# Optimization experiments

Measured on AMD Instinct MI355X. Metric: run time of the kernel, lower is better.

## Reference

```python
import jax, jax.numpy as jnp
import numpy as np

NUM_CLASSES = 2
THRESHOLD = 0.35
NEGPOS_RATIO = 7
VARIANCES = (0.1, 0.2)
B, P, O = 64, 16800, 64  # batch, num_priors, num_objs per image


def point_form(pr):
    # cxcywh -> xyxy
    return jnp.concatenate([pr[:, :2] - pr[:, 2:] / 2, pr[:, :2] + pr[:, 2:] / 2], axis=1)


def jaccard(a, b):
    # a: [A,4] xyxy, b: [Bx,4] xyxy -> IoU [A,Bx]
    lt = jnp.maximum(a[:, None, :2], b[None, :, :2])
    rb = jnp.minimum(a[:, None, 2:], b[None, :, 2:])
    wh = jnp.clip(rb - lt, 0.0)
    inter = wh[..., 0] * wh[..., 1]
    area_a = ((a[:, 2] - a[:, 0]) * (a[:, 3] - a[:, 1]))[:, None]
    area_b = ((b[:, 2] - b[:, 0]) * (b[:, 3] - b[:, 1]))[None, :]
    return inter / (area_a + area_b - inter)


def encode(matched, priors):
    # matched xyxy [P,4], priors cxcywh [P,4]
    g_cxcy = (matched[:, :2] + matched[:, 2:]) / 2 - priors[:, :2]
    g_cxcy = g_cxcy / (VARIANCES[0] * priors[:, 2:])
    g_wh = (matched[:, 2:] - matched[:, :2]) / priors[:, 2:]
    g_wh = jnp.log(g_wh) / VARIANCES[1]
    return jnp.concatenate([g_cxcy, g_wh], axis=1)


def encode_landm(matched, priors):
    # matched [P,10] -> [P,5,2]
    m = matched.reshape(-1, 5, 2)
    g = (m - priors[:, None, :2]) / (VARIANCES[0] * priors[:, None, 2:])
    return g.reshape(-1, 10)


def match_one(truths, labels, landms, priors):
    # truths [O,4], labels [O], landms [O,10]
    overlaps = jaccard(truths, point_form(priors))  # [O,P]
    best_prior_overlap = overlaps.max(axis=1)       # per-gt best IoU
    best_prior_idx = overlaps.argmax(axis=1)
    valid_gt = best_prior_overlap >= 0.2
    best_truth_overlap = overlaps.max(axis=0)       # per-prior best IoU
    best_truth_idx = overlaps.argmax(axis=0)
    # index_fill(2) only for valid gts (best_prior_idx_filter)
    bto = best_truth_overlap.at[best_prior_idx].set(
        jnp.where(valid_gt, 2.0, best_truth_overlap[best_prior_idx]))
    # ensure every gt keeps its best prior
    bti = best_truth_idx.at[best_prior_idx].set(jnp.arange(truths.shape[0]))
    matches = truths[bti]                  # [P,4]
    conf = labels[bti]                     # [P]
    conf = jnp.where(bto < THRESHOLD, 0.0, conf)
    loc = encode(matches, priors)
    landm = encode_landm(landms[bti], priors)
    return loc, conf, landm


def smooth_l1_sum(x, mask):
    ax = jnp.abs(x)
    v = jnp.where(ax < 1.0, 0.5 * ax * ax, ax - 0.5)
    return (v * mask).sum()


def setup_inputs() -> dict:
    key = jax.random.key(0)
    k1, k2, k3, k4, k5, k6, k7, k8 = jax.random.split(key, 8)
    loc_data = jax.random.normal(k1, (B, P, 4), jnp.float32)
    conf_data = jax.random.normal(k2, (B, P, NUM_CLASSES), jnp.float32)
    landm_data = jax.random.normal(k3, (B, P, 10), jnp.float32)
    # priors: cx,cy in (0,1), w,h in (0.02,0.22)
    cxy = jax.random.uniform(k4, (P, 2), jnp.float32)
    wh = jax.random.uniform(k5, (P, 2), jnp.float32) * 0.2 + 0.02
    priors = jnp.concatenate([cxy, wh], axis=1)
    # targets: valid corner boxes + landmarks + label in {1,-1}
    xy1 = jax.random.uniform(k6, (B, O, 2), jnp.float32) * 0.6
    bwh = jax.random.uniform(k7, (B, O, 2), jnp.float32) * 0.3 + 0.05
    boxes = jnp.concatenate([xy1, xy1 + bwh], axis=-1)
    lms = jax.random.uniform(k8, (B, O, 10), jnp.float32)
    lab = jnp.where(jax.random.uniform(jax.random.fold_in(key, 9), (B, O, 1)) < 0.3, -1.0, 1.0)
    targets = jnp.concatenate([boxes, lms, lab], axis=-1)
    return {"loc_data": loc_data, "conf_data": conf_data, "landm_data": landm_data,
            "priors": priors, "targets": targets}


def reference(loc_data, conf_data, landm_data, priors, targets):
    num = loc_data.shape[0]
    num_priors = priors.shape[0]
    truths = targets[:, :, :4]
    landms = targets[:, :, 4:14]
    labels = targets[:, :, -1]
    loc_t, conf_t, landm_t = jax.vmap(match_one, in_axes=(0, 0, 0, None))(
        truths, labels, landms, priors)  # [B,P,4], [B,P], [B,P,10]

    # landmark loss over conf_t > 0
    pos1 = conf_t > 0
    num_pos_landm = pos1.astype(jnp.int32).sum(axis=1, keepdims=True)
    N1 = jnp.maximum(num_pos_landm.sum().astype(jnp.float32), 1.0)
    loss_landm = smooth_l1_sum(landm_data - landm_t, pos1[..., None].astype(landm_data.dtype))

    # localization loss over conf_t != 0 ; conf_t[pos] = 1
    pos = conf_t != 0
    conf_t01 = jnp.where(pos, 1, 0)  # int {0,1}
    loss_l = smooth_l1_sum(loc_data - loc_t, pos[..., None].astype(loc_data.dtype))

    # hard negative mining on per-prior CE loss (global-max log_sum_exp, as in source)
    batch_conf = conf_data.reshape(-1, NUM_CLASSES)
    x_max = batch_conf.max()
    lse = jnp.log(jnp.exp(batch_conf - x_max).sum(axis=1, keepdims=True)) + x_max
    gathered = jnp.take_along_axis(batch_conf, conf_t01.reshape(-1, 1), axis=1)
    loss_c = (lse - gathered).reshape(num, -1)  # [B,P]; positives NOT zeroed (as in source)
    loss_idx = jnp.argsort(-loss_c, axis=1)
    idx_rank = jnp.argsort(loss_idx, axis=1)
    num_pos = pos.astype(jnp.int32).sum(axis=1, keepdims=True)  # [B,1]
    num_neg = jnp.minimum(NEGPOS_RATIO * num_pos, num_priors - 1)
    neg = idx_rank < num_neg  # [B,P]
    neg_pos = pos | neg

    # cross-entropy (sum) over selected pos+neg priors
    logp = jax.nn.log_softmax(conf_data, axis=-1)  # [B,P,C]
    ce = -jnp.take_along_axis(logp, conf_t01[..., None], axis=-1)[..., 0]
    loss_c_final = (ce * neg_pos.astype(ce.dtype)).sum()

    N = jnp.maximum(num_pos.sum().astype(jnp.float32), 1.0)
    return (loss_l / N, loss_c_final / N, loss_landm / N1)
```

## Files before the change

kernel.cpp:

```cpp
#include <hip/hip_runtime.h>
#include <math.h>

#define BN 64
#define PN 16800
#define ON 64
#define THRESH 0.35f
#define NEGPOS 7
#define GX 66
#define NBLK (BN * GX)
#define GXB 17
#define PT 4
#define TG 4

__device__ __forceinline__ unsigned f2key(float f) {
  unsigned u = __float_as_uint(f);
  return (u & 0x80000000u) ? ~u : (u | 0x80000000u);
}
__device__ __forceinline__ float key2f(unsigned k) {
  unsigned u = (k & 0x80000000u) ? (k & 0x7FFFFFFFu) : ~k;
  return __uint_as_float(u);
}
__device__ __forceinline__ float sl1(float d) {
  float a = fabsf(d);
  return (a < 1.f) ? 0.5f * a * a : a - 0.5f;
}

__global__ void k_best_truth(const float* __restrict__ priors,
                             const float* __restrict__ targets,
                             float* __restrict__ bto, int* __restrict__ bti) {
  int b = blockIdx.y;
  int tid = threadIdx.x;
  int base = blockIdx.x * 1024 + tid;

  __shared__ float4 tbox[ON];
  __shared__ float tarea[ON];
  if (tid < ON) {
    const float* tg = &targets[((long)b * ON + tid) * 15];
    float4 bx = make_float4(tg[0], tg[1], tg[2], tg[3]);
    tbox[tid] = bx;
    tarea[tid] = (bx.z - bx.x) * (bx.w - bx.y);
  }
  __syncthreads();

  float px1[PT], py1[PT], px2[PT], py2[PT], ab[PT];
  bool val[PT];
#pragma unroll
  for (int i = 0; i < PT; i++) {
    int p = base + 256 * i;
    val[i] = p < PN;
    float4 pr = reinterpret_cast<const float4*>(priors)[val[i] ? p : base];
    px1[i] = pr.x - pr.z * 0.5f; py1[i] = pr.y - pr.w * 0.5f;
    px2[i] = pr.x + pr.z * 0.5f; py2[i] = pr.y + pr.w * 0.5f;
    ab[i] = (px2[i] - px1[i]) * (py2[i] - py1[i]);
  }
  float bi[PT], bu[PT]; int id[PT];
#pragma unroll
  for (int i = 0; i < PT; i++) { bi[i] = -1.f; bu[i] = 1.f; id[i] = 0; }

#pragma unroll 4
  for (int t = 0; t < ON; t++) {
    float4 a = tbox[t];
    float aa = tarea[t];
#pragma unroll
    for (int i = 0; i < PT; i++) {
      float lx = fmaxf(a.x, px1[i]), ly = fmaxf(a.y, py1[i]);
      float rx = fminf(a.z, px2[i]), ry = fminf(a.w, py2[i]);
      float w = fmaxf(rx - lx, 0.f), h = fmaxf(ry - ly, 0.f);
      float inter = w * h;
      float uni = aa + ab[i] - inter;
      if (inter * bu[i] > bi[i] * uni) { bi[i] = inter; bu[i] = uni; id[i] = t; }
    }
  }
#pragma unroll
  for (int i = 0; i < PT; i++) {
    if (val[i]) {
      int p = base + 256 * i;
      bto[(long)b * PN + p] = bi[i] / bu[i];
      bti[(long)b * PN + p] = id[i];
    }
  }
}

__global__ void k_best_prior(const float* __restrict__ priors,
                             const float* __restrict__ targets,
                             float* __restrict__ bpo, int* __restrict__ bpi) {
  int bx = blockIdx.x;
  int b = bx >> 4;
  int t0 = (bx & 15) * TG;
  int tid = threadIdx.x;
  float ax1[TG], ay1[TG], ax2[TG], ay2[TG], area_a[TG];
#pragma unroll
  for (int i = 0; i < TG; i++) {
    const float* tg = &targets[((long)b * ON + t0 + i) * 15];
    ax1[i] = tg[0]; ay1[i] = tg[1]; ax2[i] = tg[2]; ay2[i] = tg[3];
    area_a[i] = (ax2[i] - ax1[i]) * (ay2[i] - ay1[i]);
  }
  float bi[TG], bu[TG]; int bp[TG];
#pragma unroll
  for (int i = 0; i < TG; i++) { bi[i] = -1.f; bu[i] = 1.f; bp[i] = 0x7FFFFFFF; }
  for (int p = tid; p < PN; p += 256) {
    float4 pr = reinterpret_cast<const float4*>(priors)[p];
    float px1 = pr.x - pr.z * 0.5f, py1 = pr.y - pr.w * 0.5f;
    float px2 = pr.x + pr.z * 0.5f, py2 = pr.y + pr.w * 0.5f;
    float area_b = (px2 - px1) * (py2 - py1);
#pragma unroll
    for (int i = 0; i < TG; i++) {
      float lx = fmaxf(ax1[i], px1), ly = fmaxf(ay1[i], py1);
      float rx = fminf(ax2[i], px2), ry = fminf(ay2[i], py2);
      float w = fmaxf(rx - lx, 0.f), h = fmaxf(ry - ly, 0.f);
      float inter = w * h;
      float uni = area_a[i] + area_b - inter;
      if (inter * bu[i] > bi[i] * uni) { bi[i] = inter; bu[i] = uni; bp[i] = p; }
    }
  }
#pragma unroll
  for (int off = 1; off < 64; off <<= 1) {
#pragma unroll
    for (int i = 0; i < TG; i++) {
      float oi = __shfl_xor(bi[i], off), ou = __shfl_xor(bu[i], off);
      int op = __shfl_xor(bp[i], off);
      float a = oi * bu[i], c = bi[i] * ou;
      if (a > c || (a == c && op < bp[i])) { bi[i] = oi; bu[i] = ou; bp[i] = op; }
    }
  }
  __shared__ float si[TG][4], su[TG][4];
  __shared__ int spx[TG][4];
  int w = tid >> 6;
  if ((tid & 63) == 0) {
#pragma unroll
    for (int i = 0; i < TG; i++) { si[i][w] = bi[i]; su[i][w] = bu[i]; spx[i][w] = bp[i]; }
  }
  __syncthreads();
  if (tid < TG) {
    float fi = si[tid][0], fu = su[tid][0]; int fp = spx[tid][0];
    for (int ww = 1; ww < 4; ww++) {
      float a = si[tid][ww] * fu, c = fi * su[tid][ww];
      if (a > c || (a == c && spx[tid][ww] < fp)) { fi = si[tid][ww]; fu = su[tid][ww]; fp = spx[tid][ww]; }
    }
    bpo[(long)b * ON + t0 + tid] = fi / fu;
    bpi[(long)b * ON + t0 + tid] = fp;
  }
}

__global__ void k_scatter(const float* __restrict__ bpo, const int* __restrict__ bpi,
                          float* __restrict__ bto, int* __restrict__ bti) {
  int tid = threadIdx.x;
  int row = blockIdx.x * 4 + (tid >> 6);
  int t = tid & 63;
  int q = bpi[row * ON + t];
  bool valid = bpo[row * ON + t] >= 0.2f;
  bool dupLater = false;
  for (int j = 0; j < 64; j++) {
    int ij = __shfl(q, j);
    if (j > t && ij == q) dupLater = true;
  }
  if (!dupLater) {
    bti[(long)row * PN + q] = t;
    if (valid) bto[(long)row * PN + q] = 2.0f;
  }
}

__global__ void k_encode(const float* __restrict__ loc_data,
                         const float* __restrict__ conf_data,
                         const float* __restrict__ landm_data,
                         const float* __restrict__ priors,
                         const float* __restrict__ targets,
                         const float* __restrict__ bto, const int* __restrict__ bti,
                         float* __restrict__ lossc, unsigned char* __restrict__ posf,
                         float* __restrict__ part_l, float* __restrict__ part_lm,
                         int* __restrict__ np_part, int* __restrict__ np1_part) {
  int b = blockIdx.y;
  int p = blockIdx.x * 256 + threadIdx.x;
  int bid = b * GX + blockIdx.x;
  __shared__ float4 tgs4[ON * 15 / 4];
  float* tgs = (float*)tgs4;
  if (threadIdx.x < ON * 15 / 4)
    tgs4[threadIdx.x] = reinterpret_cast<const float4*>(targets + (long)b * ON * 15)[threadIdx.x];
  __syncthreads();
  float sum_l = 0.f, sum_lm = 0.f;
  int cp = 0, cp1 = 0;
  if (p < PN) {
    int t = bti[b * PN + p];
    float ov = bto[b * PN + p];
    const float* tg = &tgs[t * 15];
    float label = tg[14];
    bool pos = ov >= THRESH;
    bool pos1 = pos && (label > 0.f);
    float4 pr = reinterpret_cast<const float4*>(priors)[p];
    if (pos) {
      float rz = 1.0f / pr.z, rw = 1.0f / pr.w;
      float m0 = tg[0], m1 = tg[1], m2 = tg[2], m3 = tg[3];
      float g0 = ((m0 + m2) * 0.5f - pr.x) * rz * 10.f;
      float g1 = ((m1 + m3) * 0.5f - pr.y) * rw * 10.f;
      float g2 = __logf((m2 - m0) * rz) * 5.f;
      float g3 = __logf((m3 - m1) * rw) * 5.f;
      const float* ld = &loc_data[((long)b * PN + p) * 4];
      sum_l = sl1(ld[0] - g0) + sl1(ld[1] - g1) + sl1(ld[2] - g2) + sl1(ld[3] - g3);
      cp = 1;
      if (pos1) {
        const float* lm = &landm_data[((long)b * PN + p) * 10];
#pragma unroll
        for (int i = 0; i < 5; i++) {
          float gx = (tg[4 + 2 * i] - pr.x) * rz * 10.f;
          float gy = (tg[5 + 2 * i] - pr.y) * rw * 10.f;
          sum_lm += sl1(lm[2 * i] - gx) + sl1(lm[2 * i + 1] - gy);
        }
        cp1 = 1;
      }
    }
    float2 c2 = reinterpret_cast<const float2*>(conf_data)[(long)b * PN + p];
    float m = fmaxf(c2.x, c2.y);
    float lse = m + __logf(__expf(c2.x - m) + __expf(c2.y - m));
    lossc[b * PN + p] = lse - (pos ? c2.y : c2.x);
    posf[b * PN + p] = pos ? 1 : 0;
  }
  for (int off = 32; off; off >>= 1) {
    sum_l += __shfl_down(sum_l, off);
    sum_lm += __shfl_down(sum_lm, off);
    cp += __shfl_down(cp, off);
    cp1 += __shfl_down(cp1, off);
  }
  __shared__ float sl4[4], slm4[4];
  __shared__ int sp4[4], sp14[4];
  int w = threadIdx.x >> 6;
  if ((threadIdx.x & 63) == 0) { sl4[w] = sum_l; slm4[w] = sum_lm; sp4[w] = cp; sp14[w] = cp1; }
  __syncthreads();
  if (threadIdx.x == 0) {
    part_l[bid] = sl4[0] + sl4[1] + sl4[2] + sl4[3];
    part_lm[bid] = slm4[0] + slm4[1] + slm4[2] + slm4[3];
    np_part[bid] = sp4[0] + sp4[1] + sp4[2] + sp4[3];
    np1_part[bid] = sp14[0] + sp14[1] + sp14[2] + sp14[3];
  }
}

__global__ void __launch_bounds__(1024) k_select(const float* __restrict__ lossc,
                                                 const unsigned char* __restrict__ posf,
                                                 const int* __restrict__ np_part,
                                                 float* __restrict__ part_c) {
  int b = blockIdx.x;
  int tid = threadIdx.x;
  __shared__ unsigned hist[256];
  __shared__ unsigned wtot[4];
  __shared__ unsigned s_d, s_rem;
  __shared__ int s_np;
  const float* row = &lossc[(long)b * PN];
  const unsigned char* prow = &posf[(long)b * PN];

  if (tid == 0) s_np = 0;
  __syncthreads();
  if (tid < GX) atomicAdd(&s_np, np_part[b * GX + tid]);
  __syncthreads();
  int k = NEGPOS * s_np;
  if (k > PN - 1) k = PN - 1;
  bool haveNeg = (k > 0);

  unsigned T = 0, R = 0, C = 0;
  if (haveNeg) {
    unsigned rem = (unsigned)k, prefix = 0;
    for (int pass = 0; pass < 4; pass++) {
      int shift = 24 - pass * 8;
      if (tid < 256) hist[tid] = 0;
      __syncthreads();
      unsigned hmask = (pass == 0) ? 0u : (0xFFFFFFFFu << (shift + 8));
      for (int p = tid; p < PN; p += 1024) {
        unsigned key = f2key(row[p]);
        if (((key ^ prefix) & hmask) == 0)
          atomicAdd(&hist[(key >> shift) & 255], 1u);
      }
      __syncthreads();
      unsigned h = (tid < 256) ? hist[tid] : 0;
      unsigned v = h;
      int lane = tid & 63;
#pragma unroll
      for (int off = 1; off < 64; off <<= 1) {
        unsigned tv = (unsigned)__shfl_down((int)v, off);
        if (lane + off < 64) v += tv;
      }
      if (tid < 256 && lane == 0) wtot[tid >> 6] = v;
      __syncthreads();
      if (tid < 256) {
        unsigned add = 0;
        for (int w2 = (tid >> 6) + 1; w2 < 4; w2++) add += wtot[w2];
        unsigned suf = v + add;
        if (suf >= rem && (suf - h) < rem) { s_d = (unsigned)tid; s_rem = rem - (suf - h); }
      }
      __syncthreads();
      prefix |= s_d << shift;
      rem = s_rem;
      if (pass == 3) { T = prefix; R = rem; C = hist[s_d]; }
      __syncthreads();
    }
  }

  float acc = 0.f;
  unsigned ptc = 0;
  for (int p = tid; p < PN; p += 1024) {
    float v = row[p];
    bool pos = prow[p] != 0;
    unsigned key = f2key(v);
    if (pos) acc += v;
    else if (haveNeg && key > T) acc += v;
    if (haveNeg && pos && key == T) ptc++;
  }
  if (haveNeg && C != R && tid < 64) {
    unsigned running = 0;
    for (int base = 0; base < PN; base += 64) {
      int p = base + tid;
      bool tie = false, pos = false;
      float v = 0.f;
      if (p < PN) { v = row[p]; tie = (f2key(v) == T); pos = prow[p] != 0; }
      unsigned long long m = __ballot(tie);
      if (tie) {
        unsigned rank = running + (unsigned)__popcll(m & ((1ull << tid) - 1));
        if (rank < R && !pos) acc += v;
      }
      running += (unsigned)__popcll(m);
    }
  }
  for (int off = 32; off; off >>= 1) {
    acc += __shfl_down(acc, off);
    ptc += __shfl_down(ptc, off);
  }
  __shared__ float wsum[16];
  __shared__ unsigned wpt[16];
  if ((tid & 63) == 0) { wsum[tid >> 6] = acc; wpt[tid >> 6] = ptc; }
  __syncthreads();
  if (tid == 0) {
    float tot = 0.f; unsigned pt = 0;
    for (int i = 0; i < 16; i++) { tot += wsum[i]; pt += wpt[i]; }
    if (haveNeg && C == R) tot += (float)(C - pt) * key2f(T);
    part_c[b] = tot;
  }
}

__global__ void k_final(const float* __restrict__ part_l, const float* __restrict__ part_lm,
                        const float* __restrict__ part_c,
                        const int* __restrict__ np_part, const int* __restrict__ np1_part,
                        float* __restrict__ out) {
  float sl = 0.f, slm = 0.f, sc = 0.f;
  int np = 0, np1 = 0;
  for (int i = threadIdx.x; i < NBLK; i += 256) {
    sl += part_l[i]; slm += part_lm[i];
    np += np_part[i]; np1 += np1_part[i];
  }
  if (threadIdx.x < BN) sc = part_c[threadIdx.x];
  for (int off = 32; off; off >>= 1) {
    sl += __shfl_down(sl, off); slm += __shfl_down(slm, off); sc += __shfl_down(sc, off);
    np += __shfl_down(np, off); np1 += __shfl_down(np1, off);
  }
  __shared__ float a[4], bsh[4], c[4];
  __shared__ int d[4], e[4];
  int w = threadIdx.x >> 6;
  if ((threadIdx.x & 63) == 0) { a[w] = sl; bsh[w] = slm; c[w] = sc; d[w] = np; e[w] = np1; }
  __syncthreads();
  if (threadIdx.x == 0) {
    float N = fmaxf((float)(d[0] + d[1] + d[2] + d[3]), 1.f);
    float N1 = fmaxf((float)(e[0] + e[1] + e[2] + e[3]), 1.f);
    out[0] = (a[0] + a[1] + a[2] + a[3]) / N;
    out[1] = (c[0] + c[1] + c[2] + c[3]) / N;
    out[2] = (bsh[0] + bsh[1] + bsh[2] + bsh[3]) / N1;
  }
}

extern "C" void kernel_launch(void* const* d_in, const int* in_sizes, int n_in,
                              void* d_out, int out_size, void* d_ws, size_t ws_size,
                              hipStream_t stream) {
  const float* loc_data = (const float*)d_in[0];
  const float* conf_data = (const float*)d_in[1];
  const float* landm_data = (const float*)d_in[2];
  const float* priors = (const float*)d_in[3];
  const float* targets = (const float*)d_in[4];
  float* out = (float*)d_out;

  char* ws = (char*)d_ws;
  const size_t SZ = (size_t)BN * PN * 4;
  size_t off = 0;
  float* lossc = (float*)(ws + off); off += SZ;
  float* bto = (float*)(ws + off); off += SZ;
  int* bti = (int*)(ws + off); off += SZ;
  unsigned char* posf = (unsigned char*)(ws + off); off += (size_t)BN * PN;
  off = (off + 15) & ~(size_t)15;
  float* bpo = (float*)(ws + off); off += (size_t)BN * ON * 4;
  int* bpi = (int*)(ws + off); off += (size_t)BN * ON * 4;
  float* part_l = (float*)(ws + off); off += NBLK * 4;
  float* part_lm = (float*)(ws + off); off += NBLK * 4;
  float* part_c = (float*)(ws + off); off += BN * 4;
  int* np_part = (int*)(ws + off); off += NBLK * 4;
  int* np1_part = (int*)(ws + off); off += NBLK * 4;

  dim3 gbt(GXB, BN);
  dim3 gbp(GX, BN);

  k_best_truth<<<gbt, 256, 0, stream>>>(priors, targets, bto, bti);
  k_best_prior<<<BN * (ON / TG), 256, 0, stream>>>(priors, targets, bpo, bpi);
  k_scatter<<<16, 256, 0, stream>>>(bpo, bpi, bto, bti);
  k_encode<<<gbp, 256, 0, stream>>>(loc_data, conf_data, landm_data, priors, targets,
                                    bto, bti, lossc, posf,
                                    part_l, part_lm, np_part, np1_part);
  k_select<<<BN, 1024, 0, stream>>>(lossc, posf, np_part, part_c);
  k_final<<<1, 256, 0, stream>>>(part_l, part_lm, part_c, np_part, np1_part, out);
}
```

Baseline: 222.7 us.

## Fold scatter into encode, cache loss keys in registers, fuse final reduction

The scatter kernel is removed. Each encode block now reads the per-gt best-prior indices and applies the overrides through a shared-memory atomicMax table, keeping the last-gt-wins and valid-flag semantics. k_select loads its row of loss keys into registers once, so the four radix passes and the final sum no longer re-read global memory. The final reduction moves into k_select using global atomics and a last-block ticket, which removes two launches but makes the float sums order-dependent and uses more registers in a 1024-thread block.

```diff
diff --git a/kernel.cpp b/kernel.cpp
--- a/kernel.cpp
+++ b/kernel.cpp
@@ -11,6 +11,15 @@
 #define GXB 17
 #define PT 4
 #define TG 4
+#define KREG 17
+#define TAILV (PN - 16 * 1024)
+
+struct GAcc {
+  unsigned ticket;
+  float sl, slm, sc;
+  int np, np1;
+  unsigned pad0, pad1;
+};
 
 __device__ __forceinline__ unsigned f2key(float f) {
   unsigned u = __float_as_uint(f);
@@ -27,10 +36,13 @@
 
 __global__ void k_best_truth(const float* __restrict__ priors,
                              const float* __restrict__ targets,
-                             float* __restrict__ bto, int* __restrict__ bti) {
+                             float* __restrict__ bto, int* __restrict__ bti,
+                             GAcc* __restrict__ gacc) {
   int b = blockIdx.y;
   int tid = threadIdx.x;
   int base = blockIdx.x * 1024 + tid;
+  if (blockIdx.x == 0 && b == 0 && tid < 8)
+    ((unsigned*)gacc)[tid] = 0;
 
   __shared__ float4 tbox[ON];
   __shared__ float tarea[ON];
@@ -142,30 +154,13 @@
   }
 }
 
-__global__ void k_scatter(const float* __restrict__ bpo, const int* __restrict__ bpi,
-                          float* __restrict__ bto, int* __restrict__ bti) {
-  int tid = threadIdx.x;
-  int row = blockIdx.x * 4 + (tid >> 6);
-  int t = tid & 63;
-  int q = bpi[row * ON + t];
-  bool valid = bpo[row * ON + t] >= 0.2f;
-  bool dupLater = false;
-  for (int j = 0; j < 64; j++) {
-    int ij = __shfl(q, j);
-    if (j > t && ij == q) dupLater = true;
-  }
-  if (!dupLater) {
-    bti[(long)row * PN + q] = t;
-    if (valid) bto[(long)row * PN + q] = 2.0f;
-  }
-}
-
 __global__ void k_encode(const float* __restrict__ loc_data,
                          const float* __restrict__ conf_data,
                          const float* __restrict__ landm_data,
                          const float* __restrict__ priors,
                          const float* __restrict__ targets,
                          const float* __restrict__ bto, const int* __restrict__ bti,
+                         const float* __restrict__ bpo, const int* __restrict__ bpi,
                          float* __restrict__ lossc, unsigned char* __restrict__ posf,
                          float* __restrict__ part_l, float* __restrict__ part_lm,
                          int* __restrict__ np_part, int* __restrict__ np1_part) {
@@ -173,15 +168,30 @@
   int p = blockIdx.x * 256 + threadIdx.x;
   int bid = b * GX + blockIdx.x;
   __shared__ float4 tgs4[ON * 15 / 4];
+  __shared__ int ovr[256];
   float* tgs = (float*)tgs4;
   if (threadIdx.x < ON * 15 / 4)
     tgs4[threadIdx.x] = reinterpret_cast<const float4*>(targets + (long)b * ON * 15)[threadIdx.x];
-  __syncthreads();
+  ovr[threadIdx.x] = -1;
+  __syncthreads();
+  if (threadIdx.x < ON) {
+    int t = threadIdx.x;
+    int q = bpi[b * ON + t];
+    int s = blockIdx.x * 256;
+    if (q >= s && q < s + 256) {
+      int valid = (bpo[b * ON + t] >= 0.2f) ? 1 : 0;
+      atomicMax(&ovr[q - s], (t << 1) | valid);
+    }
+  }
+  __syncthreads();
+
   float sum_l = 0.f, sum_lm = 0.f;
   int cp = 0, cp1 = 0;
   if (p < PN) {
     int t = bti[b * PN + p];
     float ov = bto[b * PN + p];
+    int o = ovr[threadIdx.x];
+    if (o >= 0) { t = o >> 1; if (o & 1) ov = 2.0f; }
     const float* tg = &tgs[t * 15];
     float label = tg[14];
     bool pos = ov >= THRESH;
@@ -236,7 +246,11 @@
 __global__ void __launch_bounds__(1024) k_select(const float* __restrict__ lossc,
                                                  const unsigned char* __restrict__ posf,
                                                  const int* __restrict__ np_part,
-                                                 float* __restrict__ part_c) {
+                                                 const int* __restrict__ np1_part,
+                                                 const float* __restrict__ part_l,
+                                                 const float* __restrict__ part_lm,
+                                                 GAcc* __restrict__ gacc,
+                                                 float* __restrict__ out) {
   int b = blockIdx.x;
   int tid = threadIdx.x;
   __shared__ unsigned hist[256];
@@ -250,9 +264,15 @@
   __syncthreads();
   if (tid < GX) atomicAdd(&s_np, np_part[b * GX + tid]);
   __syncthreads();
-  int k = NEGPOS * s_np;
+  int np = s_np;
+  int k = NEGPOS * np;
   if (k > PN - 1) k = PN - 1;
   bool haveNeg = (k > 0);
+
+  unsigned kreg[KREG];
+#pragma unroll
+  for (int r = 0; r < KREG - 1; r++) kreg[r] = f2key(row[tid + 1024 * r]);
+  kreg[KREG - 1] = (tid < TAILV) ? f2key(row[tid + 1024 * (KREG - 1)]) : 0u;
 
   unsigned T = 0, R = 0, C = 0;
   if (haveNeg) {
@@ -262,10 +282,13 @@
       if (tid < 256) hist[tid] = 0;
       __syncthreads();
       unsigned hmask = (pass == 0) ? 0u : (0xFFFFFFFFu << (shift + 8));
-      for (int p = tid; p < PN; p += 1024) {
-        unsigned key = f2key(row[p]);
-        if (((key ^ prefix) & hmask) == 0)
-          atomicAdd(&hist[(key >> shift) & 255], 1u);
+#pragma unroll
+      for (int r = 0; r < KREG; r++) {
+        if (r < KREG - 1 || tid < TAILV) {
+          unsigned key = kreg[r];
+          if (((key ^ prefix) & hmask) == 0)
+            atomicAdd(&hist[(key >> shift) & 255], 1u);
+        }
       }
       __syncthreads();
       unsigned h = (tid < 256) ? hist[tid] : 0;
@@ -294,13 +317,16 @@
 
   float acc = 0.f;
   unsigned ptc = 0;
-  for (int p = tid; p < PN; p += 1024) {
-    float v = row[p];
-    bool pos = prow[p] != 0;
-    unsigned key = f2key(v);
-    if (pos) acc += v;
-    else if (haveNeg && key > T) acc += v;
-    if (haveNeg && pos && key == T) ptc++;
+#pragma unroll
+  for (int r = 0; r < KREG; r++) {
+    if (r < KREG - 1 || tid < TAILV) {
+      unsigned key = kreg[r];
+      bool pos = prow[tid + 1024 * r] != 0;
+      float v = key2f(key);
+      if (pos) acc += v;
+      else if (haveNeg && key > T) acc += v;
+      if (haveNeg && pos && key == T) ptc++;
+    }
   }
   if (haveNeg && C != R && tid < 64) {
     unsigned running = 0;
@@ -325,40 +351,44 @@
   __shared__ unsigned wpt[16];
   if ((tid & 63) == 0) { wsum[tid >> 6] = acc; wpt[tid >> 6] = ptc; }
   __syncthreads();
+
+  __shared__ float s_rsl, s_rslm;
+  __shared__ int s_rnp1;
+  if (tid == 0) { s_rsl = 0.f; s_rslm = 0.f; s_rnp1 = 0; }
+  __syncthreads();
+  if (tid < GX) {
+    atomicAdd(&s_rsl, part_l[b * GX + tid]);
+    atomicAdd(&s_rslm, part_lm[b * GX + tid]);
+    atomicAdd(&s_rnp1, np1_part[b * GX + tid]);
+  }
+  __syncthreads();
+
   if (tid == 0) {
     float tot = 0.f; unsigned pt = 0;
     for (int i = 0; i < 16; i++) { tot += wsum[i]; pt += wpt[i]; }
     if (haveNeg && C == R) tot += (float)(C - pt) * key2f(T);
-    part_c[b] = tot;
-  }
-}
-
-__global__ void k_final(const float* __restrict__ part_l, const float* __restrict__ part_lm,
-                        const float* __restrict__ part_c,
-                        const int* __restrict__ np_part, const int* __restrict__ np1_part,
-                        float* __restrict__ out) {
-  float sl = 0.f, slm = 0.f, sc = 0.f;
-  int np = 0, np1 = 0;
-  for (int i = threadIdx.x; i < NBLK; i += 256) {
-    sl += part_l[i]; slm += part_lm[i];
-    np += np_part[i]; np1 += np1_part[i];
-  }
-  if (threadIdx.x < BN) sc = part_c[threadIdx.x];
-  for (int off = 32; off; off >>= 1) {
-    sl += __shfl_down(sl, off); slm += __shfl_down(slm, off); sc += __shfl_down(sc, off);
-    np += __shfl_down(np, off); np1 += __shfl_down(np1, off);
-  }
-  __shared__ float a[4], bsh[4], c[4];
-  __shared__ int d[4], e[4];
-  int w = threadIdx.x >> 6;
-  if ((threadIdx.x & 63) == 0) { a[w] = sl; bsh[w] = slm; c[w] = sc; d[w] = np; e[w] = np1; }
-  __syncthreads();
-  if (threadIdx.x == 0) {
-    float N = fmaxf((float)(d[0] + d[1] + d[2] + d[3]), 1.f);
-    float N1 = fmaxf((float)(e[0] + e[1] + e[2] + e[3]), 1.f);
-    out[0] = (a[0] + a[1] + a[2] + a[3]) / N;
-    out[1] = (c[0] + c[1] + c[2] + c[3]) / N;
-    out[2] = (bsh[0] + bsh[1] + bsh[2] + bsh[3]) / N1;
+    atomicAdd(&gacc->sc, tot);
+    atomicAdd(&gacc->sl, s_rsl);
+    atomicAdd(&gacc->slm, s_rslm);
+    atomicAdd(&gacc->np, np);
+    atomicAdd(&gacc->np1, s_rnp1);
+  }
+  __threadfence();
+  __shared__ int lastF;
+  if (tid == 0) lastF = (atomicAdd(&gacc->ticket, 1u) == (unsigned)(BN - 1)) ? 1 : 0;
+  __syncthreads();
+  if (lastF && tid == 0) {
+    __threadfence();
+    float sl = atomicAdd(&gacc->sl, 0.f);
+    float slm = atomicAdd(&gacc->slm, 0.f);
+    float sc = atomicAdd(&gacc->sc, 0.f);
+    int tnp = atomicAdd(&gacc->np, 0);
+    int tnp1 = atomicAdd(&gacc->np1, 0);
+    float N = fmaxf((float)tnp, 1.f);
+    float N1 = fmaxf((float)tnp1, 1.f);
+    out[0] = sl / N;
+    out[1] = sc / N;
+    out[2] = slm / N1;
   }
 }
 
@@ -384,19 +414,18 @@
   int* bpi = (int*)(ws + off); off += (size_t)BN * ON * 4;
   float* part_l = (float*)(ws + off); off += NBLK * 4;
   float* part_lm = (float*)(ws + off); off += NBLK * 4;
-  float* part_c = (float*)(ws + off); off += BN * 4;
   int* np_part = (int*)(ws + off); off += NBLK * 4;
   int* np1_part = (int*)(ws + off); off += NBLK * 4;
+  GAcc* gacc = (GAcc*)(ws + off); off += sizeof(GAcc);
 
   dim3 gbt(GXB, BN);
   dim3 gbp(GX, BN);
 
-  k_best_truth<<<gbt, 256, 0, stream>>>(priors, targets, bto, bti);
+  k_best_truth<<<gbt, 256, 0, stream>>>(priors, targets, bto, bti, gacc);
   k_best_prior<<<BN * (ON / TG), 256, 0, stream>>>(priors, targets, bpo, bpi);
-  k_scatter<<<16, 256, 0, stream>>>(bpo, bpi, bto, bti);
   k_encode<<<gbp, 256, 0, stream>>>(loc_data, conf_data, landm_data, priors, targets,
-                                    bto, bti, lossc, posf,
+                                    bto, bti, bpo, bpi, lossc, posf,
                                     part_l, part_lm, np_part, np1_part);
-  k_select<<<BN, 1024, 0, stream>>>(lossc, posf, np_part, part_c);
-  k_final<<<1, 256, 0, stream>>>(part_l, part_lm, part_c, np_part, np1_part, out);
-}
+  k_select<<<BN, 1024, 0, stream>>>(lossc, posf, np_part, np1_part, part_l, part_lm,
+                                    gacc, out);
+}
```

Result: slower. 232.4 us (+4.4%).
